# Kernel tuning notes

Measured on AMD Instinct MI355X. Metric: run time of the kernel, lower is better.

## Reference

```python
import jax, jax.numpy as jnp
import numpy as np

H = 16          # ATTENTION_HEAD
E = 300         # EXPANSION_LENGTH
D = 768         # TEXT_EMBEDDING_DIM
HD = D // H     # 48


def setup_inputs() -> dict:
    key = jax.random.key(0)
    ks = jax.random.split(key, 10)
    b, n, ql, kl = 1, 4, 64, 64
    q = jax.random.normal(ks[0], (b, n, ql, D), dtype=jnp.float32)
    k = jax.random.normal(ks[1], (b, 1, kl, D), dtype=jnp.float32)
    v = jax.random.normal(ks[2], (b, 1, kl, D), dtype=jnp.float32)
    s = 1.0 / np.sqrt(D)
    Wq = jax.random.normal(ks[3], (D, D), dtype=jnp.float32) * s
    bq = jnp.zeros((D,), dtype=jnp.float32)
    Wk = jax.random.normal(ks[4], (D, D), dtype=jnp.float32) * s
    bk = jnp.zeros((D,), dtype=jnp.float32)
    Wv = jax.random.normal(ks[5], (D, D), dtype=jnp.float32) * s
    bv = jnp.zeros((D,), dtype=jnp.float32)
    memory = jax.random.normal(ks[6], (1, E, H, HD), dtype=jnp.float32) * 0.05
    return {"q": q, "k": k, "v": v, "Wq": Wq, "bq": bq, "Wk": Wk,
            "bk": bk, "Wv": Wv, "bv": bv, "memory": memory}


def reference(q, k, v, Wq, bq, Wk, bk, Wv, bv, memory):
    b, n, ql, _ = q.shape
    kl = k.shape[2]
    # Dense projections
    Q = (q @ Wq + bq).reshape(b, n, ql, H, HD)          # bnqhd
    K = (k @ Wk + bk).reshape(b, kl, H, HD)             # bkhd
    V = (v @ Wv + bv).reshape(b, kl, H, HD)             # bkhd
    # memory (1,E,H,HD) -> (1,E,1,H,HD); K -> (b,1,kl,H,HD); broadcast sum
    broad_sum = memory[:, :, None, :, :] + K[:, None, :, :, :]   # bekhd
    M = jax.nn.relu(jnp.einsum('bekhd,bnqhd->bnekqh', broad_sum, Q))
    E_seq = jnp.einsum('bnekqh,bkhd->bnekhd', M, V)
    out = jnp.einsum('bnekhd,bnekqh->bnqhd', E_seq, M)
    return out.reshape(q.shape)
```

## Files before the change

kernel.cpp:

```cpp
#include <hip/hip_runtime.h>

#define H   16
#define E   300
#define D   768
#define HD  48
#define QL  64
#define KL  64
#define NH  64
#define ROWS 384
#define SPLITK 12
#define NCH 16

#define OFF_PP 0
#define OFF_PF (SPLITK*ROWS*D)
#define OFF_A  (OFF_PF + ROWS*D)
#define OFF_B  (OFF_A + NH*E*QL)
#define OFF_SP (OFF_B + NH*KL*QL)

__global__ __launch_bounds__(256, 1) void proj_kernel(
    const float* __restrict__ qin, const float* __restrict__ kin, const float* __restrict__ vin,
    const float* __restrict__ Wq, const float* __restrict__ Wk, const float* __restrict__ Wv,
    float* __restrict__ ws)
{
    const int rowblk = blockIdx.x;
    const int col0   = blockIdx.y * 128;
    const int ks     = blockIdx.z;
    const int kbase  = ks * 64;

    const int g0 = rowblk * 128;
    const float* Wlo = (g0      < 256) ? Wq : (g0      < 320) ? Wk : Wv;
    const float* Whi = (g0 + 64 < 256) ? Wq : (g0 + 64 < 320) ? Wk : Wv;

    __shared__ float XsT[32][132];
    __shared__ float Ws2[2][32][128];

    const int tid = threadIdx.x;
    const int r0  = (tid >> 4) * 8;
    const int c0  = (tid & 15) * 8;
    const int hw  = r0 >> 6;

    float acc[8][8];
    #pragma unroll
    for (int i = 0; i < 8; i++)
        #pragma unroll
        for (int j = 0; j < 8; j++) acc[i][j] = 0.f;

    for (int kk2 = 0; kk2 < 64; kk2 += 32) {
        #pragma unroll
        for (int it = 0; it < 4; it++) {
            const int idx = it * 256 + tid;
            const int row = idx >> 3;
            const int d4  = (idx & 7) * 4;
            const int grow = rowblk * 128 + row;
            const float* src = (grow < 256) ? (qin + grow * D)
                             : (grow < 320) ? (kin + (grow - 256) * D)
                                            : (vin + (grow - 320) * D);
            const float4 xv = *(const float4*)(src + kbase + kk2 + d4);
            XsT[d4 + 0][row] = xv.x; XsT[d4 + 1][row] = xv.y;
            XsT[d4 + 2][row] = xv.z; XsT[d4 + 3][row] = xv.w;
        }
        #pragma unroll
        for (int it = 0; it < 8; it++) {
            const int idx  = it * 256 + tid;
            const int half = idx >> 10;
            const int rem  = idx & 1023;
            const int dk   = rem >> 5;
            const int c4   = (rem & 31) * 4;
            const float* Wsel = half ? Whi : Wlo;
            *(float4*)&Ws2[half][dk][c4] =
                *(const float4*)(Wsel + (kbase + kk2 + dk) * D + col0 + c4);
        }
        __syncthreads();
        #pragma unroll
        for (int dk = 0; dk < 32; dk++) {
            const float4 x0 = *(const float4*)&XsT[dk][r0];
            const float4 x1 = *(const float4*)&XsT[dk][r0 + 4];
            const float4 w0 = *(const float4*)&Ws2[hw][dk][c0];
            const float4 w1 = *(const float4*)&Ws2[hw][dk][c0 + 4];
            const float xr[8] = {x0.x, x0.y, x0.z, x0.w, x1.x, x1.y, x1.z, x1.w};
            const float wc[8] = {w0.x, w0.y, w0.z, w0.w, w1.x, w1.y, w1.z, w1.w};
            #pragma unroll
            for (int i = 0; i < 8; i++)
                #pragma unroll
                for (int j = 0; j < 8; j++)
                    acc[i][j] = fmaf(xr[i], wc[j], acc[i][j]);
        }
        __syncthreads();
    }
    float* P = ws + OFF_PP + ks * (ROWS * D);
    #pragma unroll
    for (int i = 0; i < 8; i++) {
        float* base = P + (rowblk * 128 + r0 + i) * D + col0 + c0;
        *(float4*)(base)     = make_float4(acc[i][0], acc[i][1], acc[i][2], acc[i][3]);
        *(float4*)(base + 4) = make_float4(acc[i][4], acc[i][5], acc[i][6], acc[i][7]);
    }
}

__global__ __launch_bounds__(256) void reduce_kernel(
    const float* __restrict__ bq, const float* __restrict__ bk, const float* __restrict__ bv,
    float* __restrict__ ws)
{
    const int idx = (blockIdx.x * 256 + threadIdx.x) * 4;
    const float* PP = ws + OFF_PP;
    float4 v = *(const float4*)(PP + idx);
    #pragma unroll
    for (int c = 1; c < SPLITK; c++) {
        const float4 p = *(const float4*)(PP + c * (ROWS * D) + idx);
        v.x += p.x; v.y += p.y; v.z += p.z; v.w += p.w;
    }
    const int row = idx / D, col = idx % D;
    const float* bias = (row < 256) ? bq : (row < 320) ? bk : bv;
    const float4 b = *(const float4*)(bias + col);
    v.x += b.x; v.y += b.y; v.z += b.z; v.w += b.w;
    *(float4*)(ws + OFF_PF + idx) = v;
}

__global__ __launch_bounds__(256) void ab_kernel(
    const float* __restrict__ memo, float* __restrict__ ws)
{
    const int nh = blockIdx.x;
    const int rg = blockIdx.y;
    const int n = nh >> 4, h = nh & 15;
    const float* Pf = ws + OFF_PF;
    float* A = ws + OFF_A;
    float* B = ws + OFF_B;

    __shared__ float RsT[48][132];
    __shared__ float QsT[48][68];

    const int tid = threadIdx.x;
    #pragma unroll
    for (int it = 0; it < 6; it++) {
        const int idx = it * 256 + tid;
        const int row = idx / 12;
        const int d4  = (idx % 12) * 4;
        const int rr = rg * 128 + row;
        float4 rv = make_float4(0.f, 0.f, 0.f, 0.f);
        if (rr < E)            rv = *(const float4*)(memo + rr * D + h * HD + d4);
        else if (rr < E + KL)  rv = *(const float4*)(Pf + (256 + rr - E) * D + h * HD + d4);
        RsT[d4 + 0][row] = rv.x; RsT[d4 + 1][row] = rv.y;
        RsT[d4 + 2][row] = rv.z; RsT[d4 + 3][row] = rv.w;
    }
    #pragma unroll
    for (int it = 0; it < 3; it++) {
        const int idx = it * 256 + tid;
        const int q  = idx / 12;
        const int d4 = (idx % 12) * 4;
        const float4 qv = *(const float4*)(Pf + (n * QL + q) * D + h * HD + d4);
        QsT[d4 + 0][q] = qv.x; QsT[d4 + 1][q] = qv.y;
        QsT[d4 + 2][q] = qv.z; QsT[d4 + 3][q] = qv.w;
    }
    __syncthreads();

    const int r0 = (tid >> 4) * 8;
    const int q0 = (tid & 15) * 4;
    float acc[8][4];
    #pragma unroll
    for (int i = 0; i < 8; i++)
        #pragma unroll
        for (int j = 0; j < 4; j++) acc[i][j] = 0.f;

    #pragma unroll 4
    for (int d = 0; d < HD; d++) {
        const float4 rf0 = *(const float4*)&RsT[d][r0];
        const float4 rf1 = *(const float4*)&RsT[d][r0 + 4];
        const float4 qf  = *(const float4*)&QsT[d][q0];
        const float rr8[8] = {rf0.x, rf0.y, rf0.z, rf0.w, rf1.x, rf1.y, rf1.z, rf1.w};
        const float qq4[4] = {qf.x, qf.y, qf.z, qf.w};
        #pragma unroll
        for (int i = 0; i < 8; i++)
            #pragma unroll
            for (int j = 0; j < 4; j++)
                acc[i][j] = fmaf(rr8[i], qq4[j], acc[i][j]);
    }
    #pragma unroll
    for (int i = 0; i < 8; i++) {
        const int rr = rg * 128 + r0 + i;
        const float4 av = make_float4(acc[i][0], acc[i][1], acc[i][2], acc[i][3]);
        if (rr < E)            *(float4*)(A + (nh * E + rr) * QL + q0) = av;
        else if (rr < E + KL)  *(float4*)(B + (nh * KL + (rr - E)) * QL + q0) = av;
    }
}

__global__ __launch_bounds__(256, 1) void main_kernel(float* __restrict__ ws)
{
    const int nh = blockIdx.x;
    const int cg = blockIdx.y;
    const int tid = threadIdx.x;
    const int lane = tid & 63;
    const int w = tid >> 6;

    __shared__ float As[75 * 64];
    __shared__ float Bs[64][68];

    const float* Ag = ws + OFF_A + (nh * E + cg * 75) * QL;
    for (int idx = tid; idx < 1200; idx += 256)
        *(float4*)&As[idx * 4] = *(const float4*)(Ag + idx * 4);
    const float* Bg = ws + OFF_B + nh * (KL * QL);
    #pragma unroll
    for (int it = 0; it < 4; it++) {
        const int idx = it * 256 + tid;
        const int k  = idx >> 4;
        const int q4 = (idx & 15) * 4;
        *(float4*)&Bs[k][q4] = *(const float4*)(Bg + idx * 4);
    }
    __syncthreads();

    float b[64];
    #pragma unroll
    for (int j = 0; j < 16; j++)
        *(float4*)&b[j * 4] = *(const float4*)&Bs[lane][j * 4];

    float s[64];
    #pragma unroll
    for (int j = 0; j < 64; j++) s[j] = 0.f;

    const int eBeg = w * 19;
    const int eEnd = (eBeg + 19 < 75) ? eBeg + 19 : 75;
    for (int e = eBeg; e < eEnd; e++) {
        float m[64];
        #pragma unroll
        for (int j4 = 0; j4 < 16; j4++) {
            const float4 a = *(const float4*)&As[e * 64 + j4 * 4];
            m[j4 * 4 + 0] = fmaxf(a.x + b[j4 * 4 + 0], 0.f);
            m[j4 * 4 + 1] = fmaxf(a.y + b[j4 * 4 + 1], 0.f);
            m[j4 * 4 + 2] = fmaxf(a.z + b[j4 * 4 + 2], 0.f);
            m[j4 * 4 + 3] = fmaxf(a.w + b[j4 * 4 + 3], 0.f);
        }
        float p0 = 0.f, p1 = 0.f, p2 = 0.f, p3 = 0.f;
        #pragma unroll
        for (int j4 = 0; j4 < 16; j4++) {
            p0 += m[j4 * 4 + 0]; p1 += m[j4 * 4 + 1];
            p2 += m[j4 * 4 + 2]; p3 += m[j4 * 4 + 3];
        }
        const float p = (p0 + p1) + (p2 + p3);
        #pragma unroll
        for (int j = 0; j < 64; j++)
            s[j] = fmaf(m[j], p, s[j]);
    }

    float* Sp = ws + OFF_SP + (((cg * 4 + w) * NH + nh) * QL) * KL;
    #pragma unroll
    for (int q = 0; q < 64; q++)
        Sp[q * KL + lane] = s[q];
}

__global__ __launch_bounds__(256) void out_kernel(
    const float* __restrict__ ws_c, float* __restrict__ outp)
{
    const int nh = blockIdx.x;
    const int qq = blockIdx.y;
    const int n = nh >> 4, h = nh & 15;
    const int q0 = qq * 16;
    const float* Sp = ws_c + OFF_SP;
    const float* Pf = ws_c + OFF_PF;

    __shared__ float S_l[16][64];
    __shared__ float V_l[64][52];

    const int tid = threadIdx.x;
    #pragma unroll
    for (int it = 0; it < 4; it++) {
        const int idx = it * 256 + tid;
        const int qi = idx >> 6, k = idx & 63;
        float sum = 0.f;
        #pragma unroll
        for (int c = 0; c < NCH; c++)
            sum += Sp[((c * NH + nh) * QL + q0 + qi) * KL + k];
        S_l[qi][k] = sum;
    }
    #pragma unroll
    for (int it = 0; it < 3; it++) {
        const int idx = it * 256 + tid;
        const int k  = idx / 12;
        const int d4 = (idx % 12) * 4;
        *(float4*)&V_l[k][d4] = *(const float4*)(Pf + (320 + k) * D + h * HD + d4);
    }
    __syncthreads();

    const int qi = tid >> 4;
    const int dg = tid & 15;
    if (dg < 12) {
        float a0 = 0.f, a1 = 0.f, a2 = 0.f, a3 = 0.f;
        #pragma unroll 8
        for (int k = 0; k < KL; k++) {
            const float sv = S_l[qi][k];
            const float4 vf = *(const float4*)&V_l[k][dg * 4];
            a0 = fmaf(sv, vf.x, a0); a1 = fmaf(sv, vf.y, a1);
            a2 = fmaf(sv, vf.z, a2); a3 = fmaf(sv, vf.w, a3);
        }
        *(float4*)(outp + (n * QL + q0 + qi) * D + h * HD + dg * 4) =
            make_float4(a0, a1, a2, a3);
    }
}

extern "C" void kernel_launch(void* const* d_in, const int* in_sizes, int n_in,
                              void* d_out, int out_size, void* d_ws, size_t ws_size,
                              hipStream_t stream)
{
    const float* q    = (const float*)d_in[0];
    const float* k    = (const float*)d_in[1];
    const float* v    = (const float*)d_in[2];
    const float* Wq   = (const float*)d_in[3];
    const float* bq   = (const float*)d_in[4];
    const float* Wk   = (const float*)d_in[5];
    const float* bk   = (const float*)d_in[6];
    const float* Wv   = (const float*)d_in[7];
    const float* bv   = (const float*)d_in[8];
    const float* memo = (const float*)d_in[9];
    float* ws   = (float*)d_ws;
    float* outp = (float*)d_out;

    hipLaunchKernelGGL(proj_kernel, dim3(3, 6, 12), dim3(256), 0, stream,
                       q, k, v, Wq, Wk, Wv, ws);
    hipLaunchKernelGGL(reduce_kernel, dim3(288), dim3(256), 0, stream, bq, bk, bv, ws);
    hipLaunchKernelGGL(ab_kernel, dim3(64, 3), dim3(256), 0, stream, memo, ws);
    hipLaunchKernelGGL(main_kernel, dim3(64, 4), dim3(256), 0, stream, ws);
    hipLaunchKernelGGL(out_kernel, dim3(64, 4), dim3(256), 0, stream, ws, outp);
}
```

Measured before the change: 124.2 us.

## Fuse five kernels into one persistent kernel with software grid barriers

Replaces the five separate launches (projection, split-K reduce, A/B compute, main, output) with a single 256-block kernel whose stages are separated by atomic-counter grid barriers, with shared memory reused through a union. The goal is to remove the launch overhead and idle gaps between the small kernels. In exchange it adds a memset launch plus spin-wait barriers, and it relies on all 256 blocks being co-resident. Launch bounds also change to allow two blocks per CU, which may tighten register budgets for the main stage's large per-thread arrays.

```diff
diff --git a/kernel.cpp b/kernel.cpp
--- a/kernel.cpp
+++ b/kernel.cpp
@@ -10,287 +10,300 @@
 #define ROWS 384
 #define SPLITK 12
 #define NCH 16
+#define NBLK 256
 
 #define OFF_PP 0
 #define OFF_PF (SPLITK*ROWS*D)
 #define OFF_A  (OFF_PF + ROWS*D)
 #define OFF_B  (OFF_A + NH*E*QL)
 #define OFF_SP (OFF_B + NH*KL*QL)
-
-__global__ __launch_bounds__(256, 1) void proj_kernel(
+#define OFF_BAR (OFF_SP + NCH*NH*QL*KL)
+
+union SharedU {
+    struct { float XsT[32][132]; float Ws2[2][32][128]; } p1;
+    struct { float RsT[48][132]; float QsT[48][68]; } p3;
+    struct { float As[75 * 64]; float Bs[64][68]; } p4;
+    struct { float S_l[16][64]; float V_l[64][52]; } p5;
+};
+
+__device__ __forceinline__ void grid_barrier(unsigned* __restrict__ bar, int site)
+{
+    __syncthreads();
+    if (threadIdx.x == 0) {
+        __threadfence();
+        const unsigned arrived = atomicAdd(&bar[site], 1u) + 1u;
+        if (arrived < NBLK) {
+            while (atomicAdd(&bar[site], 0u) < NBLK)
+                __builtin_amdgcn_s_sleep(8);
+        }
+        __threadfence();
+    }
+    __syncthreads();
+}
+
+__global__ __launch_bounds__(256, 2) void fused_kernel(
     const float* __restrict__ qin, const float* __restrict__ kin, const float* __restrict__ vin,
     const float* __restrict__ Wq, const float* __restrict__ Wk, const float* __restrict__ Wv,
-    float* __restrict__ ws)
+    const float* __restrict__ bq, const float* __restrict__ bk, const float* __restrict__ bv,
+    const float* __restrict__ memo, float* __restrict__ ws, float* __restrict__ outp)
 {
-    const int rowblk = blockIdx.x;
-    const int col0   = blockIdx.y * 128;
-    const int ks     = blockIdx.z;
-    const int kbase  = ks * 64;
-
-    const int g0 = rowblk * 128;
-    const float* Wlo = (g0      < 256) ? Wq : (g0      < 320) ? Wk : Wv;
-    const float* Whi = (g0 + 64 < 256) ? Wq : (g0 + 64 < 320) ? Wk : Wv;
-
-    __shared__ float XsT[32][132];
-    __shared__ float Ws2[2][32][128];
-
+    __shared__ SharedU sh;
+    unsigned* bar = (unsigned*)(ws + OFF_BAR);
+    const int bid = blockIdx.x;
     const int tid = threadIdx.x;
-    const int r0  = (tid >> 4) * 8;
-    const int c0  = (tid & 15) * 8;
-    const int hw  = r0 >> 6;
-
-    float acc[8][8];
-    #pragma unroll
-    for (int i = 0; i < 8; i++)
-        #pragma unroll
-        for (int j = 0; j < 8; j++) acc[i][j] = 0.f;
-
-    for (int kk2 = 0; kk2 < 64; kk2 += 32) {
-        #pragma unroll
-        for (int it = 0; it < 4; it++) {
-            const int idx = it * 256 + tid;
-            const int row = idx >> 3;
-            const int d4  = (idx & 7) * 4;
-            const int grow = rowblk * 128 + row;
-            const float* src = (grow < 256) ? (qin + grow * D)
-                             : (grow < 320) ? (kin + (grow - 256) * D)
-                                            : (vin + (grow - 320) * D);
-            const float4 xv = *(const float4*)(src + kbase + kk2 + d4);
-            XsT[d4 + 0][row] = xv.x; XsT[d4 + 1][row] = xv.y;
-            XsT[d4 + 2][row] = xv.z; XsT[d4 + 3][row] = xv.w;
-        }
-        #pragma unroll
-        for (int it = 0; it < 8; it++) {
-            const int idx  = it * 256 + tid;
-            const int half = idx >> 10;
-            const int rem  = idx & 1023;
-            const int dk   = rem >> 5;
-            const int c4   = (rem & 31) * 4;
-            const float* Wsel = half ? Whi : Wlo;
-            *(float4*)&Ws2[half][dk][c4] =
-                *(const float4*)(Wsel + (kbase + kk2 + dk) * D + col0 + c4);
+
+    if (bid < 216) {
+        const int rowblk = bid / 72;
+        const int colblk = (bid % 72) / 12;
+        const int ks     = bid % 12;
+        const int col0   = colblk * 128;
+        const int kbase  = ks * 64;
+
+        const int g0 = rowblk * 128;
+        const float* Wlo = (g0      < 256) ? Wq : (g0      < 320) ? Wk : Wv;
+        const float* Whi = (g0 + 64 < 256) ? Wq : (g0 + 64 < 320) ? Wk : Wv;
+
+        const int r0 = (tid >> 4) * 8;
+        const int c0 = (tid & 15) * 8;
+        const int hw = r0 >> 6;
+
+        float acc[8][8];
+        #pragma unroll
+        for (int i = 0; i < 8; i++)
+            #pragma unroll
+            for (int j = 0; j < 8; j++) acc[i][j] = 0.f;
+
+        for (int kk2 = 0; kk2 < 64; kk2 += 32) {
+            #pragma unroll
+            for (int it = 0; it < 4; it++) {
+                const int idx = it * 256 + tid;
+                const int row = idx >> 3;
+                const int d4  = (idx & 7) * 4;
+                const int grow = rowblk * 128 + row;
+                const float* src = (grow < 256) ? (qin + grow * D)
+                                 : (grow < 320) ? (kin + (grow - 256) * D)
+                                                : (vin + (grow - 320) * D);
+                const float4 xv = *(const float4*)(src + kbase + kk2 + d4);
+                sh.p1.XsT[d4 + 0][row] = xv.x; sh.p1.XsT[d4 + 1][row] = xv.y;
+                sh.p1.XsT[d4 + 2][row] = xv.z; sh.p1.XsT[d4 + 3][row] = xv.w;
+            }
+            #pragma unroll
+            for (int it = 0; it < 8; it++) {
+                const int idx  = it * 256 + tid;
+                const int half = idx >> 10;
+                const int rem  = idx & 1023;
+                const int dk   = rem >> 5;
+                const int c4   = (rem & 31) * 4;
+                const float* Wsel = half ? Whi : Wlo;
+                *(float4*)&sh.p1.Ws2[half][dk][c4] =
+                    *(const float4*)(Wsel + (kbase + kk2 + dk) * D + col0 + c4);
+            }
+            __syncthreads();
+            #pragma unroll
+            for (int dk = 0; dk < 32; dk++) {
+                const float4 x0 = *(const float4*)&sh.p1.XsT[dk][r0];
+                const float4 x1 = *(const float4*)&sh.p1.XsT[dk][r0 + 4];
+                const float4 w0 = *(const float4*)&sh.p1.Ws2[hw][dk][c0];
+                const float4 w1 = *(const float4*)&sh.p1.Ws2[hw][dk][c0 + 4];
+                const float xr[8] = {x0.x, x0.y, x0.z, x0.w, x1.x, x1.y, x1.z, x1.w};
+                const float wc[8] = {w0.x, w0.y, w0.z, w0.w, w1.x, w1.y, w1.z, w1.w};
+                #pragma unroll
+                for (int i = 0; i < 8; i++)
+                    #pragma unroll
+                    for (int j = 0; j < 8; j++)
+                        acc[i][j] = fmaf(xr[i], wc[j], acc[i][j]);
+            }
+            __syncthreads();
+        }
+        float* P = ws + OFF_PP + ks * (ROWS * D);
+        #pragma unroll
+        for (int i = 0; i < 8; i++) {
+            float* base = P + (rowblk * 128 + r0 + i) * D + col0 + c0;
+            *(float4*)(base)     = make_float4(acc[i][0], acc[i][1], acc[i][2], acc[i][3]);
+            *(float4*)(base + 4) = make_float4(acc[i][4], acc[i][5], acc[i][6], acc[i][7]);
+        }
+    }
+    grid_barrier(bar, 0);
+
+    for (int j = bid; j < 288; j += NBLK) {
+        const int idx = (j * 256 + tid) * 4;
+        const float* PP = ws + OFF_PP;
+        float4 acc4 = *(const float4*)(PP + idx);
+        #pragma unroll
+        for (int c = 1; c < SPLITK; c++) {
+            const float4 p = *(const float4*)(PP + c * (ROWS * D) + idx);
+            acc4.x += p.x; acc4.y += p.y; acc4.z += p.z; acc4.w += p.w;
+        }
+        const int row = idx / D, col = idx % D;
+        const float* bias = (row < 256) ? bq : (row < 320) ? bk : bv;
+        const float4 bb = *(const float4*)(bias + col);
+        acc4.x += bb.x; acc4.y += bb.y; acc4.z += bb.z; acc4.w += bb.w;
+        *(float4*)(ws + OFF_PF + idx) = acc4;
+    }
+    grid_barrier(bar, 1);
+
+    if (bid < 192) {
+        const int nh = bid & 63;
+        const int rg = bid >> 6;
+        const int n = nh >> 4, h = nh & 15;
+        const float* Pf = ws + OFF_PF;
+        float* A = ws + OFF_A;
+        float* B = ws + OFF_B;
+
+        #pragma unroll
+        for (int it = 0; it < 6; it++) {
+            const int idx = it * 256 + tid;
+            const int row = idx / 12;
+            const int d4  = (idx % 12) * 4;
+            const int rr = rg * 128 + row;
+            float4 rv = make_float4(0.f, 0.f, 0.f, 0.f);
+            if (rr < E)            rv = *(const float4*)(memo + rr * D + h * HD + d4);
+            else if (rr < E + KL)  rv = *(const float4*)(Pf + (256 + rr - E) * D + h * HD + d4);
+            sh.p3.RsT[d4 + 0][row] = rv.x; sh.p3.RsT[d4 + 1][row] = rv.y;
+            sh.p3.RsT[d4 + 2][row] = rv.z; sh.p3.RsT[d4 + 3][row] = rv.w;
+        }
+        #pragma unroll
+        for (int it = 0; it < 3; it++) {
+            const int idx = it * 256 + tid;
+            const int q  = idx / 12;
+            const int d4 = (idx % 12) * 4;
+            const float4 qv = *(const float4*)(Pf + (n * QL + q) * D + h * HD + d4);
+            sh.p3.QsT[d4 + 0][q] = qv.x; sh.p3.QsT[d4 + 1][q] = qv.y;
+            sh.p3.QsT[d4 + 2][q] = qv.z; sh.p3.QsT[d4 + 3][q] = qv.w;
         }
         __syncthreads();
-        #pragma unroll
-        for (int dk = 0; dk < 32; dk++) {
-            const float4 x0 = *(const float4*)&XsT[dk][r0];
-            const float4 x1 = *(const float4*)&XsT[dk][r0 + 4];
-            const float4 w0 = *(const float4*)&Ws2[hw][dk][c0];
-            const float4 w1 = *(const float4*)&Ws2[hw][dk][c0 + 4];
-            const float xr[8] = {x0.x, x0.y, x0.z, x0.w, x1.x, x1.y, x1.z, x1.w};
-            const float wc[8] = {w0.x, w0.y, w0.z, w0.w, w1.x, w1.y, w1.z, w1.w};
+
+        const int r0 = (tid >> 4) * 8;
+        const int q0 = (tid & 15) * 4;
+        float acc[8][4];
+        #pragma unroll
+        for (int i = 0; i < 8; i++)
+            #pragma unroll
+            for (int j = 0; j < 4; j++) acc[i][j] = 0.f;
+
+        #pragma unroll 4
+        for (int d = 0; d < HD; d++) {
+            const float4 rf0 = *(const float4*)&sh.p3.RsT[d][r0];
+            const float4 rf1 = *(const float4*)&sh.p3.RsT[d][r0 + 4];
+            const float4 qf  = *(const float4*)&sh.p3.QsT[d][q0];
+            const float rr8[8] = {rf0.x, rf0.y, rf0.z, rf0.w, rf1.x, rf1.y, rf1.z, rf1.w};
+            const float qq4[4] = {qf.x, qf.y, qf.z, qf.w};
             #pragma unroll
             for (int i = 0; i < 8; i++)
                 #pragma unroll
-                for (int j = 0; j < 8; j++)
-                    acc[i][j] = fmaf(xr[i], wc[j], acc[i][j]);
+                for (int j = 0; j < 4; j++)
+                    acc[i][j] = fmaf(rr8[i], qq4[j], acc[i][j]);
+        }
+        #pragma unroll
+        for (int i = 0; i < 8; i++) {
+            const int rr = rg * 128 + r0 + i;
+            const float4 av = make_float4(acc[i][0], acc[i][1], acc[i][2], acc[i][3]);
+            if (rr < E)            *(float4*)(A + (nh * E + rr) * QL + q0) = av;
+            else if (rr < E + KL)  *(float4*)(B + (nh * KL + (rr - E)) * QL + q0) = av;
+        }
+    }
+    grid_barrier(bar, 2);
+
+    {
+        const int nh = bid & 63;
+        const int eg = bid >> 6;
+        const int lane = tid & 63;
+        const int w = tid >> 6;
+
+        const float* Ag = ws + OFF_A + (nh * E + eg * 75) * QL;
+        for (int idx = tid; idx < 1200; idx += 256)
+            *(float4*)&sh.p4.As[idx * 4] = *(const float4*)(Ag + idx * 4);
+        const float* Bg = ws + OFF_B + nh * (KL * QL);
+        #pragma unroll
+        for (int it = 0; it < 4; it++) {
+            const int idx = it * 256 + tid;
+            const int k  = idx >> 4;
+            const int q4 = (idx & 15) * 4;
+            *(float4*)&sh.p4.Bs[k][q4] = *(const float4*)(Bg + idx * 4);
         }
         __syncthreads();
-    }
-    float* P = ws + OFF_PP + ks * (ROWS * D);
-    #pragma unroll
-    for (int i = 0; i < 8; i++) {
-        float* base = P + (rowblk * 128 + r0 + i) * D + col0 + c0;
-        *(float4*)(base)     = make_float4(acc[i][0], acc[i][1], acc[i][2], acc[i][3]);
-        *(float4*)(base + 4) = make_float4(acc[i][4], acc[i][5], acc[i][6], acc[i][7]);
-    }
-}
-
-__global__ __launch_bounds__(256) void reduce_kernel(
-    const float* __restrict__ bq, const float* __restrict__ bk, const float* __restrict__ bv,
-    float* __restrict__ ws)
-{
-    const int idx = (blockIdx.x * 256 + threadIdx.x) * 4;
-    const float* PP = ws + OFF_PP;
-    float4 v = *(const float4*)(PP + idx);
-    #pragma unroll
-    for (int c = 1; c < SPLITK; c++) {
-        const float4 p = *(const float4*)(PP + c * (ROWS * D) + idx);
-        v.x += p.x; v.y += p.y; v.z += p.z; v.w += p.w;
-    }
-    const int row = idx / D, col = idx % D;
-    const float* bias = (row < 256) ? bq : (row < 320) ? bk : bv;
-    const float4 b = *(const float4*)(bias + col);
-    v.x += b.x; v.y += b.y; v.z += b.z; v.w += b.w;
-    *(float4*)(ws + OFF_PF + idx) = v;
-}
-
-__global__ __launch_bounds__(256) void ab_kernel(
-    const float* __restrict__ memo, float* __restrict__ ws)
-{
-    const int nh = blockIdx.x;
-    const int rg = blockIdx.y;
-    const int n = nh >> 4, h = nh & 15;
-    const float* Pf = ws + OFF_PF;
-    float* A = ws + OFF_A;
-    float* B = ws + OFF_B;
-
-    __shared__ float RsT[48][132];
-    __shared__ float QsT[48][68];
-
-    const int tid = threadIdx.x;
-    #pragma unroll
-    for (int it = 0; it < 6; it++) {
-        const int idx = it * 256 + tid;
-        const int row = idx / 12;
-        const int d4  = (idx % 12) * 4;
-        const int rr = rg * 128 + row;
-        float4 rv = make_float4(0.f, 0.f, 0.f, 0.f);
-        if (rr < E)            rv = *(const float4*)(memo + rr * D + h * HD + d4);
-        else if (rr < E + KL)  rv = *(const float4*)(Pf + (256 + rr - E) * D + h * HD + d4);
-        RsT[d4 + 0][row] = rv.x; RsT[d4 + 1][row] = rv.y;
-        RsT[d4 + 2][row] = rv.z; RsT[d4 + 3][row] = rv.w;
-    }
-    #pragma unroll
-    for (int it = 0; it < 3; it++) {
-        const int idx = it * 256 + tid;
-        const int q  = idx / 12;
-        const int d4 = (idx % 12) * 4;
-        const float4 qv = *(const float4*)(Pf + (n * QL + q) * D + h * HD + d4);
-        QsT[d4 + 0][q] = qv.x; QsT[d4 + 1][q] = qv.y;
-        QsT[d4 + 2][q] = qv.z; QsT[d4 + 3][q] = qv.w;
-    }
-    __syncthreads();
-
-    const int r0 = (tid >> 4) * 8;
-    const int q0 = (tid & 15) * 4;
-    float acc[8][4];
-    #pragma unroll
-    for (int i = 0; i < 8; i++)
-        #pragma unroll
-        for (int j = 0; j < 4; j++) acc[i][j] = 0.f;
-
-    #pragma unroll 4
-    for (int d = 0; d < HD; d++) {
-        const float4 rf0 = *(const float4*)&RsT[d][r0];
-        const float4 rf1 = *(const float4*)&RsT[d][r0 + 4];
-        const float4 qf  = *(const float4*)&QsT[d][q0];
-        const float rr8[8] = {rf0.x, rf0.y, rf0.z, rf0.w, rf1.x, rf1.y, rf1.z, rf1.w};
-        const float qq4[4] = {qf.x, qf.y, qf.z, qf.w};
-        #pragma unroll
-        for (int i = 0; i < 8; i++)
-            #pragma unroll
-            for (int j = 0; j < 4; j++)
-                acc[i][j] = fmaf(rr8[i], qq4[j], acc[i][j]);
-    }
-    #pragma unroll
-    for (int i = 0; i < 8; i++) {
-        const int rr = rg * 128 + r0 + i;
-        const float4 av = make_float4(acc[i][0], acc[i][1], acc[i][2], acc[i][3]);
-        if (rr < E)            *(float4*)(A + (nh * E + rr) * QL + q0) = av;
-        else if (rr < E + KL)  *(float4*)(B + (nh * KL + (rr - E)) * QL + q0) = av;
-    }
-}
-
-__global__ __launch_bounds__(256, 1) void main_kernel(float* __restrict__ ws)
-{
-    const int nh = blockIdx.x;
-    const int cg = blockIdx.y;
-    const int tid = threadIdx.x;
-    const int lane = tid & 63;
-    const int w = tid >> 6;
-
-    __shared__ float As[75 * 64];
-    __shared__ float Bs[64][68];
-
-    const float* Ag = ws + OFF_A + (nh * E + cg * 75) * QL;
-    for (int idx = tid; idx < 1200; idx += 256)
-        *(float4*)&As[idx * 4] = *(const float4*)(Ag + idx * 4);
-    const float* Bg = ws + OFF_B + nh * (KL * QL);
-    #pragma unroll
-    for (int it = 0; it < 4; it++) {
-        const int idx = it * 256 + tid;
-        const int k  = idx >> 4;
-        const int q4 = (idx & 15) * 4;
-        *(float4*)&Bs[k][q4] = *(const float4*)(Bg + idx * 4);
-    }
-    __syncthreads();
-
-    float b[64];
-    #pragma unroll
-    for (int j = 0; j < 16; j++)
-        *(float4*)&b[j * 4] = *(const float4*)&Bs[lane][j * 4];
-
-    float s[64];
-    #pragma unroll
-    for (int j = 0; j < 64; j++) s[j] = 0.f;
-
-    const int eBeg = w * 19;
-    const int eEnd = (eBeg + 19 < 75) ? eBeg + 19 : 75;
-    for (int e = eBeg; e < eEnd; e++) {
-        float m[64];
-        #pragma unroll
-        for (int j4 = 0; j4 < 16; j4++) {
-            const float4 a = *(const float4*)&As[e * 64 + j4 * 4];
-            m[j4 * 4 + 0] = fmaxf(a.x + b[j4 * 4 + 0], 0.f);
-            m[j4 * 4 + 1] = fmaxf(a.y + b[j4 * 4 + 1], 0.f);
-            m[j4 * 4 + 2] = fmaxf(a.z + b[j4 * 4 + 2], 0.f);
-            m[j4 * 4 + 3] = fmaxf(a.w + b[j4 * 4 + 3], 0.f);
-        }
-        float p0 = 0.f, p1 = 0.f, p2 = 0.f, p3 = 0.f;
-        #pragma unroll
-        for (int j4 = 0; j4 < 16; j4++) {
-            p0 += m[j4 * 4 + 0]; p1 += m[j4 * 4 + 1];
-            p2 += m[j4 * 4 + 2]; p3 += m[j4 * 4 + 3];
-        }
-        const float p = (p0 + p1) + (p2 + p3);
-        #pragma unroll
-        for (int j = 0; j < 64; j++)
-            s[j] = fmaf(m[j], p, s[j]);
-    }
-
-    float* Sp = ws + OFF_SP + (((cg * 4 + w) * NH + nh) * QL) * KL;
-    #pragma unroll
-    for (int q = 0; q < 64; q++)
-        Sp[q * KL + lane] = s[q];
-}
-
-__global__ __launch_bounds__(256) void out_kernel(
-    const float* __restrict__ ws_c, float* __restrict__ outp)
-{
-    const int nh = blockIdx.x;
-    const int qq = blockIdx.y;
-    const int n = nh >> 4, h = nh & 15;
-    const int q0 = qq * 16;
-    const float* Sp = ws_c + OFF_SP;
-    const float* Pf = ws_c + OFF_PF;
-
-    __shared__ float S_l[16][64];
-    __shared__ float V_l[64][52];
-
-    const int tid = threadIdx.x;
-    #pragma unroll
-    for (int it = 0; it < 4; it++) {
-        const int idx = it * 256 + tid;
-        const int qi = idx >> 6, k = idx & 63;
-        float sum = 0.f;
-        #pragma unroll
-        for (int c = 0; c < NCH; c++)
-            sum += Sp[((c * NH + nh) * QL + q0 + qi) * KL + k];
-        S_l[qi][k] = sum;
-    }
-    #pragma unroll
-    for (int it = 0; it < 3; it++) {
-        const int idx = it * 256 + tid;
-        const int k  = idx / 12;
-        const int d4 = (idx % 12) * 4;
-        *(float4*)&V_l[k][d4] = *(const float4*)(Pf + (320 + k) * D + h * HD + d4);
-    }
-    __syncthreads();
-
-    const int qi = tid >> 4;
-    const int dg = tid & 15;
-    if (dg < 12) {
-        float a0 = 0.f, a1 = 0.f, a2 = 0.f, a3 = 0.f;
-        #pragma unroll 8
-        for (int k = 0; k < KL; k++) {
-            const float sv = S_l[qi][k];
-            const float4 vf = *(const float4*)&V_l[k][dg * 4];
-            a0 = fmaf(sv, vf.x, a0); a1 = fmaf(sv, vf.y, a1);
-            a2 = fmaf(sv, vf.z, a2); a3 = fmaf(sv, vf.w, a3);
-        }
-        *(float4*)(outp + (n * QL + q0 + qi) * D + h * HD + dg * 4) =
-            make_float4(a0, a1, a2, a3);
+
+        float b[64];
+        #pragma unroll
+        for (int j = 0; j < 16; j++)
+            *(float4*)&b[j * 4] = *(const float4*)&sh.p4.Bs[lane][j * 4];
+
+        float s[64];
+        #pragma unroll
+        for (int j = 0; j < 64; j++) s[j] = 0.f;
+
+        const int eBeg = w * 19;
+        const int eEnd = (eBeg + 19 < 75) ? eBeg + 19 : 75;
+        for (int e = eBeg; e < eEnd; e++) {
+            float m[64];
+            #pragma unroll
+            for (int j4 = 0; j4 < 16; j4++) {
+                const float4 a = *(const float4*)&sh.p4.As[e * 64 + j4 * 4];
+                m[j4 * 4 + 0] = fmaxf(a.x + b[j4 * 4 + 0], 0.f);
+                m[j4 * 4 + 1] = fmaxf(a.y + b[j4 * 4 + 1], 0.f);
+                m[j4 * 4 + 2] = fmaxf(a.z + b[j4 * 4 + 2], 0.f);
+                m[j4 * 4 + 3] = fmaxf(a.w + b[j4 * 4 + 3], 0.f);
+            }
+            float p0 = 0.f, p1 = 0.f, p2 = 0.f, p3 = 0.f;
+            #pragma unroll
+            for (int j4 = 0; j4 < 16; j4++) {
+                p0 += m[j4 * 4 + 0]; p1 += m[j4 * 4 + 1];
+                p2 += m[j4 * 4 + 2]; p3 += m[j4 * 4 + 3];
+            }
+            const float p = (p0 + p1) + (p2 + p3);
+            #pragma unroll
+            for (int j = 0; j < 64; j++)
+                s[j] = fmaf(m[j], p, s[j]);
+        }
+
+        float* Sp = ws + OFF_SP + (((eg * 4 + w) * NH + nh) * QL) * KL;
+        #pragma unroll
+        for (int q = 0; q < 64; q++)
+            Sp[q * KL + lane] = s[q];
+    }
+    grid_barrier(bar, 3);
+
+    {
+        const int nh = bid & 63;
+        const int qq = bid >> 6;
+        const int n = nh >> 4, h = nh & 15;
+        const int q0 = qq * 16;
+        const float* Sp = ws + OFF_SP;
+        const float* Pf = ws + OFF_PF;
+
+        #pragma unroll
+        for (int it = 0; it < 4; it++) {
+            const int idx = it * 256 + tid;
+            const int qi = idx >> 6, k = idx & 63;
+            float sum = 0.f;
+            #pragma unroll
+            for (int c = 0; c < NCH; c++)
+                sum += Sp[((c * NH + nh) * QL + q0 + qi) * KL + k];
+            sh.p5.S_l[qi][k] = sum;
+        }
+        #pragma unroll
+        for (int it = 0; it < 3; it++) {
+            const int idx = it * 256 + tid;
+            const int k  = idx / 12;
+            const int d4 = (idx % 12) * 4;
+            *(float4*)&sh.p5.V_l[k][d4] = *(const float4*)(Pf + (320 + k) * D + h * HD + d4);
+        }
+        __syncthreads();
+
+        const int qi = tid >> 4;
+        const int dg = tid & 15;
+        if (dg < 12) {
+            float a0 = 0.f, a1 = 0.f, a2 = 0.f, a3 = 0.f;
+            #pragma unroll 8
+            for (int k = 0; k < KL; k++) {
+                const float sv = sh.p5.S_l[qi][k];
+                const float4 vf = *(const float4*)&sh.p5.V_l[k][dg * 4];
+                a0 = fmaf(sv, vf.x, a0); a1 = fmaf(sv, vf.y, a1);
+                a2 = fmaf(sv, vf.z, a2); a3 = fmaf(sv, vf.w, a3);
+            }
+            *(float4*)(outp + (n * QL + q0 + qi) * D + h * HD + dg * 4) =
+                make_float4(a0, a1, a2, a3);
+        }
     }
 }
 
@@ -311,10 +324,8 @@
     float* ws   = (float*)d_ws;
     float* outp = (float*)d_out;
 
-    hipLaunchKernelGGL(proj_kernel, dim3(3, 6, 12), dim3(256), 0, stream,
-                       q, k, v, Wq, Wk, Wv, ws);
-    hipLaunchKernelGGL(reduce_kernel, dim3(288), dim3(256), 0, stream, bq, bk, bv, ws);
-    hipLaunchKernelGGL(ab_kernel, dim3(64, 3), dim3(256), 0, stream, memo, ws);
-    hipLaunchKernelGGL(main_kernel, dim3(64, 4), dim3(256), 0, stream, ws);
-    hipLaunchKernelGGL(out_kernel, dim3(64, 4), dim3(256), 0, stream, ws, outp);
+    hipMemsetAsync(ws + OFF_BAR, 0, 4 * sizeof(unsigned), stream);
+
+    hipLaunchKernelGGL(fused_kernel, dim3(NBLK), dim3(256), 0, stream,
+                       q, k, v, Wq, Wk, Wv, bq, bk, bv, memo, ws, outp);
 }
```

Measured after the change: 232.6 us. +87.3%, slower.

## Shrink projection tiles for more blocks and reduce main-kernel partials in shared memory

Applied to the files above, without the earlier changes.

The projection GEMM now uses 64-row tiles with a single weight matrix per block, doubling the grid to 432 blocks and allowing two blocks per CU. The main kernel now reduces its four per-wave partial score matrices through shared memory before writing one partial per block, which cuts the partial-sum buffer written by main_kernel and read by out_kernel by a factor of four (NCH goes from 16 to 4). This trades more projection blocks and extra barriers and LDS traffic against less global memory traffic.

```diff
diff --git a/kernel.cpp b/kernel.cpp
--- a/kernel.cpp
+++ b/kernel.cpp
@@ -9,7 +9,7 @@
 #define NH  64
 #define ROWS 384
 #define SPLITK 12
-#define NCH 16
+#define NCH 4
 
 #define OFF_PP 0
 #define OFF_PF (SPLITK*ROWS*D)
@@ -17,7 +17,7 @@
 #define OFF_B  (OFF_A + NH*E*QL)
 #define OFF_SP (OFF_B + NH*KL*QL)
 
-__global__ __launch_bounds__(256, 1) void proj_kernel(
+__global__ __launch_bounds__(256, 2) void proj_kernel(
     const float* __restrict__ qin, const float* __restrict__ kin, const float* __restrict__ vin,
     const float* __restrict__ Wq, const float* __restrict__ Wk, const float* __restrict__ Wv,
     float* __restrict__ ws)
@@ -27,31 +27,28 @@
     const int ks     = blockIdx.z;
     const int kbase  = ks * 64;
 
-    const int g0 = rowblk * 128;
-    const float* Wlo = (g0      < 256) ? Wq : (g0      < 320) ? Wk : Wv;
-    const float* Whi = (g0 + 64 < 256) ? Wq : (g0 + 64 < 320) ? Wk : Wv;
-
-    __shared__ float XsT[32][132];
-    __shared__ float Ws2[2][32][128];
+    const float* W = (rowblk < 4) ? Wq : (rowblk == 4) ? Wk : Wv;
+
+    __shared__ float XsT[32][68];
+    __shared__ float Ws[32][128];
 
     const int tid = threadIdx.x;
-    const int r0  = (tid >> 4) * 8;
+    const int r0  = (tid >> 4) * 4;
     const int c0  = (tid & 15) * 8;
-    const int hw  = r0 >> 6;
-
-    float acc[8][8];
-    #pragma unroll
-    for (int i = 0; i < 8; i++)
+
+    float acc[4][8];
+    #pragma unroll
+    for (int i = 0; i < 4; i++)
         #pragma unroll
         for (int j = 0; j < 8; j++) acc[i][j] = 0.f;
 
     for (int kk2 = 0; kk2 < 64; kk2 += 32) {
         #pragma unroll
-        for (int it = 0; it < 4; it++) {
+        for (int it = 0; it < 2; it++) {
             const int idx = it * 256 + tid;
             const int row = idx >> 3;
             const int d4  = (idx & 7) * 4;
-            const int grow = rowblk * 128 + row;
+            const int grow = rowblk * 64 + row;
             const float* src = (grow < 256) ? (qin + grow * D)
                              : (grow < 320) ? (kin + (grow - 256) * D)
                                             : (vin + (grow - 320) * D);
@@ -60,27 +57,23 @@
             XsT[d4 + 2][row] = xv.z; XsT[d4 + 3][row] = xv.w;
         }
         #pragma unroll
-        for (int it = 0; it < 8; it++) {
-            const int idx  = it * 256 + tid;
-            const int half = idx >> 10;
-            const int rem  = idx & 1023;
-            const int dk   = rem >> 5;
-            const int c4   = (rem & 31) * 4;
-            const float* Wsel = half ? Whi : Wlo;
-            *(float4*)&Ws2[half][dk][c4] =
-                *(const float4*)(Wsel + (kbase + kk2 + dk) * D + col0 + c4);
+        for (int it = 0; it < 4; it++) {
+            const int idx = it * 256 + tid;
+            const int dk  = idx >> 5;
+            const int c4  = (idx & 31) * 4;
+            *(float4*)&Ws[dk][c4] =
+                *(const float4*)(W + (kbase + kk2 + dk) * D + col0 + c4);
         }
         __syncthreads();
         #pragma unroll
         for (int dk = 0; dk < 32; dk++) {
             const float4 x0 = *(const float4*)&XsT[dk][r0];
-            const float4 x1 = *(const float4*)&XsT[dk][r0 + 4];
-            const float4 w0 = *(const float4*)&Ws2[hw][dk][c0];
-            const float4 w1 = *(const float4*)&Ws2[hw][dk][c0 + 4];
-            const float xr[8] = {x0.x, x0.y, x0.z, x0.w, x1.x, x1.y, x1.z, x1.w};
+            const float4 w0 = *(const float4*)&Ws[dk][c0];
+            const float4 w1 = *(const float4*)&Ws[dk][c0 + 4];
+            const float xr[4] = {x0.x, x0.y, x0.z, x0.w};
             const float wc[8] = {w0.x, w0.y, w0.z, w0.w, w1.x, w1.y, w1.z, w1.w};
             #pragma unroll
-            for (int i = 0; i < 8; i++)
+            for (int i = 0; i < 4; i++)
                 #pragma unroll
                 for (int j = 0; j < 8; j++)
                     acc[i][j] = fmaf(xr[i], wc[j], acc[i][j]);
@@ -89,8 +82,8 @@
     }
     float* P = ws + OFF_PP + ks * (ROWS * D);
     #pragma unroll
-    for (int i = 0; i < 8; i++) {
-        float* base = P + (rowblk * 128 + r0 + i) * D + col0 + c0;
+    for (int i = 0; i < 4; i++) {
+        float* base = P + (rowblk * 64 + r0 + i) * D + col0 + c0;
         *(float4*)(base)     = make_float4(acc[i][0], acc[i][1], acc[i][2], acc[i][3]);
         *(float4*)(base + 4) = make_float4(acc[i][4], acc[i][5], acc[i][6], acc[i][7]);
     }
@@ -185,31 +178,33 @@
 __global__ __launch_bounds__(256, 1) void main_kernel(float* __restrict__ ws)
 {
     const int nh = blockIdx.x;
-    const int cg = blockIdx.y;
+    const int eg = blockIdx.y;
     const int tid = threadIdx.x;
     const int lane = tid & 63;
     const int w = tid >> 6;
 
-    __shared__ float As[75 * 64];
-    __shared__ float Bs[64][68];
-
-    const float* Ag = ws + OFF_A + (nh * E + cg * 75) * QL;
+    __shared__ union {
+        struct { float As[75 * 64]; float Bs[64][68]; } a;
+        struct { float r0[64 * 64]; float r1[64 * 64]; } r;
+    } sh;
+
+    const float* Ag = ws + OFF_A + (nh * E + eg * 75) * QL;
     for (int idx = tid; idx < 1200; idx += 256)
-        *(float4*)&As[idx * 4] = *(const float4*)(Ag + idx * 4);
+        *(float4*)&sh.a.As[idx * 4] = *(const float4*)(Ag + idx * 4);
     const float* Bg = ws + OFF_B + nh * (KL * QL);
     #pragma unroll
     for (int it = 0; it < 4; it++) {
         const int idx = it * 256 + tid;
         const int k  = idx >> 4;
         const int q4 = (idx & 15) * 4;
-        *(float4*)&Bs[k][q4] = *(const float4*)(Bg + idx * 4);
+        *(float4*)&sh.a.Bs[k][q4] = *(const float4*)(Bg + idx * 4);
     }
     __syncthreads();
 
     float b[64];
     #pragma unroll
     for (int j = 0; j < 16; j++)
-        *(float4*)&b[j * 4] = *(const float4*)&Bs[lane][j * 4];
+        *(float4*)&b[j * 4] = *(const float4*)&sh.a.Bs[lane][j * 4];
 
     float s[64];
     #pragma unroll
@@ -221,7 +216,7 @@
         float m[64];
         #pragma unroll
         for (int j4 = 0; j4 < 16; j4++) {
-            const float4 a = *(const float4*)&As[e * 64 + j4 * 4];
+            const float4 a = *(const float4*)&sh.a.As[e * 64 + j4 * 4];
             m[j4 * 4 + 0] = fmaxf(a.x + b[j4 * 4 + 0], 0.f);
             m[j4 * 4 + 1] = fmaxf(a.y + b[j4 * 4 + 1], 0.f);
             m[j4 * 4 + 2] = fmaxf(a.z + b[j4 * 4 + 2], 0.f);
@@ -239,10 +234,32 @@
             s[j] = fmaf(m[j], p, s[j]);
     }
 
-    float* Sp = ws + OFF_SP + (((cg * 4 + w) * NH + nh) * QL) * KL;
-    #pragma unroll
-    for (int q = 0; q < 64; q++)
-        Sp[q * KL + lane] = s[q];
+    __syncthreads();
+    if (w >= 2) {
+        float* red = (w == 2) ? sh.r.r0 : sh.r.r1;
+        #pragma unroll
+        for (int q = 0; q < 64; q++) red[q * 64 + lane] = s[q];
+    }
+    __syncthreads();
+    if (w == 0) {
+        #pragma unroll
+        for (int q = 0; q < 64; q++) s[q] += sh.r.r0[q * 64 + lane];
+    } else if (w == 1) {
+        #pragma unroll
+        for (int q = 0; q < 64; q++) s[q] += sh.r.r1[q * 64 + lane];
+    }
+    __syncthreads();
+    if (w == 1) {
+        #pragma unroll
+        for (int q = 0; q < 64; q++) sh.r.r0[q * 64 + lane] = s[q];
+    }
+    __syncthreads();
+    if (w == 0) {
+        float* Sp = ws + OFF_SP + ((eg * NH + nh) * QL) * KL;
+        #pragma unroll
+        for (int q = 0; q < 64; q++)
+            Sp[q * KL + lane] = s[q] + sh.r.r0[q * 64 + lane];
+    }
 }
 
 __global__ __launch_bounds__(256) void out_kernel(
@@ -311,7 +328,7 @@
     float* ws   = (float*)d_ws;
     float* outp = (float*)d_out;
 
-    hipLaunchKernelGGL(proj_kernel, dim3(3, 6, 12), dim3(256), 0, stream,
+    hipLaunchKernelGGL(proj_kernel, dim3(6, 6, 12), dim3(256), 0, stream,
                        q, k, v, Wq, Wk, Wv, ws);
     hipLaunchKernelGGL(reduce_kernel, dim3(288), dim3(256), 0, stream, bq, bk, bv, ws);
     hipLaunchKernelGGL(ab_kernel, dim3(64, 3), dim3(256), 0, stream, memo, ws);
```

Measured after the change: 121.8 us. About the same (-1.9%).
